# Performance work log

Hardware: AMD Instinct MI355X
Metric: run time of the kernel (lower is better)

The kernel has to match this reference:

```python
import jax, jax.numpy as jnp
import numpy as np

DIM = 2048
N_HEADS = 16
KV_LORA = 512
NOPE = 128
ROPE = 64
V_DIM = 128
QK_DIM = NOPE + ROPE  # 192
B, S = 2, 2048
ROPE_THETA = 10000.0
ROPE_FACTOR = 40.0
BETA_FAST, BETA_SLOW = 32, 1
ORIG_LEN, MAX_LEN = 4096, 16384
MSCALE_ARG = 1.0
EPS = 1e-6


def _precompute_freqs(seqlen):
    # DeepSeek YaRN-corrected rotary frequencies (interleaved-pair convention).
    d = ROPE
    freqs = 1.0 / (ROPE_THETA ** (np.arange(0, d, 2, dtype=np.float64) / d))
    if MAX_LEN > ORIG_LEN:
        def corr_dim(n_rot):
            return d * np.log(ORIG_LEN / (n_rot * 2 * np.pi)) / (2 * np.log(ROPE_THETA))
        low = max(int(np.floor(corr_dim(BETA_FAST))), 0)
        high = min(int(np.ceil(corr_dim(BETA_SLOW))), d - 1)
        smooth = 1.0 - np.clip((np.arange(d // 2) - low) / max(high - low, 1e-3), 0, 1)
        freqs = freqs / ROPE_FACTOR * (1 - smooth) + freqs * smooth
    t = np.arange(seqlen, dtype=np.float64)
    ang = np.outer(t, freqs)  # [S, d/2]
    return np.cos(ang).astype(np.float32), np.sin(ang).astype(np.float32)


def softmax_scale():
    scale = QK_DIM ** -0.5
    if MAX_LEN > ORIG_LEN:
        m = 0.1 * MSCALE_ARG * float(np.log(ROPE_FACTOR)) + 1.0
        scale = scale * m * m
    return scale


def setup_inputs() -> dict:
    key = jax.random.key(0)
    ks = jax.random.split(key, 6)
    w_std = 0.02
    fc, fs = _precompute_freqs(S)
    return {
        "x": jax.random.normal(ks[0], (B, S, DIM), jnp.float32),
        "wq": jax.random.normal(ks[1], (N_HEADS * QK_DIM, DIM), jnp.float32) * w_std,
        "wkv_a": jax.random.normal(ks[2], (KV_LORA + ROPE, DIM), jnp.float32) * w_std,
        "kv_norm_w": jnp.ones((KV_LORA,), jnp.float32),
        "wkv_b": jax.random.normal(ks[3], (N_HEADS * (NOPE + V_DIM), KV_LORA), jnp.float32) * w_std,
        "wo": jax.random.normal(ks[4], (DIM, N_HEADS * V_DIM), jnp.float32) * w_std,
        "freqs_cos": jnp.asarray(fc),
        "freqs_sin": jnp.asarray(fs),
    }


def _apply_rotary(x, cos, sin):
    # x: [B, S, H, d]; interleaved complex pairs, cos/sin: [S, d/2]
    xr = x.reshape(*x.shape[:-1], -1, 2)
    x_re, x_im = xr[..., 0], xr[..., 1]
    c = cos[None, :, None, :]
    s = sin[None, :, None, :]
    y_re = x_re * c - x_im * s
    y_im = x_re * s + x_im * c
    return jnp.stack((y_re, y_im), axis=-1).reshape(x.shape)


def _rmsnorm(x, w):
    return x * jax.lax.rsqrt(jnp.mean(x * x, axis=-1, keepdims=True) + EPS) * w


def reference(x, wq, wkv_a, kv_norm_w, wkv_b, wo, freqs_cos, freqs_sin):
    b, s, _ = x.shape
    # Q projection (q_lora_rank == 0 path)
    q = (x @ wq.T).reshape(b, s, N_HEADS, QK_DIM)
    q_nope, q_pe = q[..., :NOPE], q[..., NOPE:]
    q_pe = _apply_rotary(q_pe, freqs_cos, freqs_sin)
    # Low-rank KV compression
    kv = x @ wkv_a.T  # [B, S, 512+64]
    kv_c, k_pe = kv[..., :KV_LORA], kv[..., KV_LORA:]
    k_pe = _apply_rotary(k_pe[:, :, None, :], freqs_cos, freqs_sin)  # [B,S,1,64]
    kv_c = _rmsnorm(kv_c, kv_norm_w)
    kvb = (kv_c @ wkv_b.T).reshape(b, s, N_HEADS, NOPE + V_DIM)
    k_nope, v = kvb[..., :NOPE], kvb[..., NOPE:]
    k = jnp.concatenate([k_nope, jnp.broadcast_to(k_pe, (b, s, N_HEADS, ROPE))], axis=-1)
    # Causal attention
    scores = jnp.einsum("bshd,bthd->bhst", q, k) * softmax_scale()
    causal = jnp.tril(jnp.ones((s, s), bool))
    scores = jnp.where(causal[None, None], scores, jnp.float32(-1e30))
    p = jax.nn.softmax(scores, axis=-1)
    out = jnp.einsum("bhst,bthd->bshd", p, v).reshape(b, s, N_HEADS * V_DIM)
    return out @ wo.T
```

## Files before the change

### kernel.cpp

```cpp
#include <hip/hip_runtime.h>
#include <math.h>

#define NH      16
#define D_NOPE  128
#define D_ROPE  64
#define D_QK    192
#define D_V     128
#define KV_LORA 512
#define NB      2
#define SEQ     2048
#define NTOK    (NB*SEQ)
#define QROW    (NH*D_QK)
#define KVBROW  (NH*(D_NOPE+D_V))
#define EPSF    1e-6f

typedef unsigned short u16;
typedef float  floatx4 __attribute__((ext_vector_type(4)));
typedef __bf16 bf16x8  __attribute__((ext_vector_type(8)));
typedef u16    u16x4   __attribute__((ext_vector_type(4)));
typedef u16    u16x8   __attribute__((ext_vector_type(8)));

__device__ __forceinline__ u16 f2bf(float f) {
    unsigned u = __builtin_bit_cast(unsigned, f);
    return (u16)((u + 0x7fffu + ((u >> 16) & 1u)) >> 16);
}

__device__ __forceinline__ void async_copy16(const void* g, void* l) {
    __builtin_amdgcn_global_load_lds(
        (const __attribute__((address_space(1))) unsigned int*)g,
        (__attribute__((address_space(3))) unsigned int*)l,
        16, 0, 0);
}

__global__ __launch_bounds__(256) void cast_all(const float* __restrict__ x,
                                                const float* __restrict__ wq,
                                                const float* __restrict__ wkva,
                                                const float* __restrict__ wkvb,
                                                const float* __restrict__ wo,
                                                u16* __restrict__ xb,
                                                u16* __restrict__ wqb,
                                                u16* __restrict__ wkvab,
                                                u16* __restrict__ wkvbb,
                                                u16* __restrict__ wob) {
    int blk = blockIdx.x;
    const float* src; u16* dst; bool pad = false;
    if (blk < 8192)        { src = x;    dst = xb; }
    else if (blk < 14336)  { blk -= 8192;  src = wq;   dst = wqb; }
    else if (blk < 15616)  { blk -= 14336; src = wkva; dst = wkvab; pad = true; }
    else if (blk < 17664)  { blk -= 15616; src = wkvb; dst = wkvbb; }
    else                   { blk -= 17664; src = wo;   dst = wob; }
    const int i = (blk * 256 + threadIdx.x) * 4;
    u16x4 o;
    if (pad && (i >> 11) >= 576) {
        o[0] = 0; o[1] = 0; o[2] = 0; o[3] = 0;
    } else {
        const float4 v = *(const float4*)&src[i];
        o[0] = f2bf(v.x); o[1] = f2bf(v.y); o[2] = f2bf(v.z); o[3] = f2bf(v.w);
    }
    *(u16x4*)&dst[i] = o;
}

template<int MODE>
__global__ __launch_bounds__(256) void gemm_mfma(const u16* __restrict__ A,
                                                 const u16* __restrict__ B,
                                                 void* __restrict__ Cout,
                                                 u16* __restrict__ kbuf,
                                                 u16* __restrict__ vT,
                                                 int M, int N, int K) {
    __shared__ u16 As[128 * 32];
    __shared__ u16 Bs[128 * 32];
    const int tid  = threadIdx.x;
    const int wave = tid >> 6, lane = tid & 63;
    const int m0 = blockIdx.y * 128, n0 = blockIdx.x * 128;
    const int wm = (wave & 1) * 64, wn = (wave >> 1) * 64;

    const int srow = wave * 32 + (lane >> 2);
    const int kch  = (lane & 3) * 8;
    const u16* gA0 = A + (size_t)(m0 + srow) * K + kch;
    const u16* gA1 = gA0 + (size_t)16 * K;
    const u16* gB0 = B + (size_t)(n0 + srow) * K + kch;
    const u16* gB1 = gB0 + (size_t)16 * K;
    u16* lA0 = &As[(wave * 32) * 32];
    u16* lA1 = &As[(wave * 32 + 16) * 32];
    u16* lB0 = &Bs[(wave * 32) * 32];
    u16* lB1 = &Bs[(wave * 32 + 16) * 32];

    floatx4 acc[4][4];
#pragma unroll
    for (int i = 0; i < 4; ++i)
#pragma unroll
        for (int j = 0; j < 4; ++j) acc[i][j] = 0.f;

    const int lrow = lane & 15;
    const int lkh  = (lane >> 4) * 8;

    for (int k0 = 0; k0 < K; k0 += 32) {
        __syncthreads();
        async_copy16(gA0 + k0, lA0);
        async_copy16(gA1 + k0, lA1);
        async_copy16(gB0 + k0, lB0);
        async_copy16(gB1 + k0, lB1);
        __syncthreads();
        bf16x8 a[4], b[4];
#pragma unroll
        for (int mi = 0; mi < 4; ++mi)
            a[mi] = *(const bf16x8*)&As[(wm + mi * 16 + lrow) * 32 + lkh];
#pragma unroll
        for (int ni = 0; ni < 4; ++ni)
            b[ni] = *(const bf16x8*)&Bs[(wn + ni * 16 + lrow) * 32 + lkh];
#pragma unroll
        for (int mi = 0; mi < 4; ++mi)
#pragma unroll
            for (int ni = 0; ni < 4; ++ni)
                acc[mi][ni] = __builtin_amdgcn_mfma_f32_16x16x32_bf16(
                    a[mi], b[ni], acc[mi][ni], 0, 0, 0);
    }

    const int crow = (lane >> 4) * 4, ccol = lane & 15;
#pragma unroll
    for (int mi = 0; mi < 4; ++mi)
#pragma unroll
        for (int ni = 0; ni < 4; ++ni) {
            const int m = m0 + wm + mi * 16 + crow;
            const int c = n0 + wn + ni * 16 + ccol;
            if (MODE == 0) {
                float* cp = (float*)Cout + (size_t)m * N + c;
#pragma unroll
                for (int r = 0; r < 4; ++r) cp[(size_t)r * N] = acc[mi][ni][r];
            } else if (MODE == 1) {
                u16* cp = (u16*)Cout + (size_t)m * N + c;
#pragma unroll
                for (int r = 0; r < 4; ++r) cp[(size_t)r * N] = f2bf(acc[mi][ni][r]);
            } else {
                const int hh = c >> 8, j = c & 255;
                const int bb = m >> 11, t = m & 2047;
                if (j < 128) {
#pragma unroll
                    for (int r = 0; r < 4; ++r)
                        kbuf[(((size_t)hh * 2 + bb) * 2048 + t + r) * 192 + j] =
                            f2bf(acc[mi][ni][r]);
                } else {
                    u16x4 pk;
#pragma unroll
                    for (int r = 0; r < 4; ++r) pk[r] = f2bf(acc[mi][ni][r]);
                    *(u16x4*)&vT[(((size_t)hh * 2 + bb) * 128 + (j - 128)) * 2048 + t] = pk;
                }
            }
        }
}


__global__ __launch_bounds__(256) void kv_fix(const float* __restrict__ kv_raw,
                                              const float* __restrict__ w,
                                              const float* __restrict__ fcos,
                                              const float* __restrict__ fsin,
                                              u16* __restrict__ kvn_bf,
                                              u16* __restrict__ kbuf) {
    const int row = blockIdx.x;
    const int tid = threadIdx.x;
    const float* src = kv_raw + (size_t)row * 640;
    const float v0 = src[tid];
    const float v1 = src[256 + tid];
    float ss = v0 * v0 + v1 * v1;
#pragma unroll
    for (int off = 32; off > 0; off >>= 1) ss += __shfl_down(ss, off, 64);
    __shared__ float red[4];
    __shared__ float kpe_s[64];
    if ((tid & 63) == 0) red[tid >> 6] = ss;
    if (tid < 32) {
        const int s = row & (SEQ - 1);
        const float c  = fcos[s * 32 + tid];
        const float sn = fsin[s * 32 + tid];
        const float xr = src[KV_LORA + 2 * tid];
        const float xi = src[KV_LORA + 2 * tid + 1];
        kpe_s[2 * tid]     = xr * c - xi * sn;
        kpe_s[2 * tid + 1] = xr * sn + xi * c;
    }
    __syncthreads();
    const float tot = red[0] + red[1] + red[2] + red[3];
    const float inv = rsqrtf(tot * (1.0f / KV_LORA) + EPSF);
    kvn_bf[(size_t)row * KV_LORA + tid]       = f2bf(v0 * inv * w[tid]);
    kvn_bf[(size_t)row * KV_LORA + 256 + tid] = f2bf(v1 * inv * w[256 + tid]);
    const int bb = row >> 11, t = row & 2047;
    const int hh = tid >> 4, dg = (tid & 15) * 4;
    u16x4 pk;
#pragma unroll
    for (int j = 0; j < 4; ++j) pk[j] = f2bf(kpe_s[dg + j]);
    *(u16x4*)&kbuf[(((size_t)hh * 2 + bb) * 2048 + t) * 192 + 128 + dg] = pk;
}

__global__ __launch_bounds__(256, 2) void attn_mfma(const u16* __restrict__ qbf,
                                                    const u16* __restrict__ kbuf,
                                                    const u16* __restrict__ vT,
                                                    u16* __restrict__ att,
                                                    float scale) {
    __shared__ __attribute__((aligned(16))) u16 Ks[6 * 64 * 32];
    __shared__ __attribute__((aligned(16))) u16 Vs[2 * 128 * 32];
    __shared__ __attribute__((aligned(16))) u16 Ps[4][32 * 72];
    const int x = blockIdx.x;
    const int qt_base = (x & 1) ? (15 - (x >> 1)) : (x >> 1);
    const int qt = blockIdx.z ? (15 - qt_base) : qt_base;
    const int h = blockIdx.y, b = blockIdx.z;
    const int tid = threadIdx.x, wave = tid >> 6, lane = tid & 63;
    const int l15 = lane & 15, lg = lane >> 4;

    const u16* kb_base = kbuf + ((size_t)(h * 2 + b)) * 2048 * 192;
    const u16* vt_base = vT   + ((size_t)(h * 2 + b)) * 128 * 2048;

    int qrow[2];
    bf16x8 qf[2][6];
#pragma unroll
    for (int g = 0; g < 2; ++g) {
        qrow[g] = qt * 128 + g * 64 + wave * 16 + l15;
        const size_t qoff = ((size_t)(b * SEQ + qrow[g])) * QROW + h * 192 + lg * 8;
#pragma unroll
        for (int s = 0; s < 6; ++s) qf[g][s] = *(const bf16x8*)&qbf[qoff + s * 32];
    }

    floatx4 oacc[2][8];
#pragma unroll
    for (int g = 0; g < 2; ++g)
#pragma unroll
        for (int v = 0; v < 8; ++v) oacc[g][v] = 0.f;
    float m_run[2] = {-1e30f, -1e30f}, l_run[2] = {0.f, 0.f};

    const int kt_max = 2 * qt + 1;
    for (int kt = 0; kt <= kt_max; ++kt) {
        const int t0 = kt * 64;
        __syncthreads();
#pragma unroll
        for (int i = 0; i < 6; ++i) {
            const int base = (wave * 6 + i) * 64;
            const int slot = base + lane;
            const int s = slot >> 8, r = slot & 255, tk = r >> 2, ch = r & 3;
            async_copy16(kb_base + ((size_t)(t0 + tk)) * 192 + s * 32 + ch * 8,
                         &Ks[base * 8]);
        }
#pragma unroll
        for (int i = 0; i < 4; ++i) {
            const int base = (wave * 4 + i) * 64;
            const int slot = base + lane;
            const int s = slot >> 9, r = slot & 511, v = r >> 2, ch = r & 3;
            async_copy16(vt_base + ((size_t)v) * 2048 + t0 + s * 32 + ch * 8,
                         &Vs[base * 8]);
        }
        __syncthreads();
        floatx4 sacc[2][4];
#pragma unroll
        for (int g = 0; g < 2; ++g)
#pragma unroll
            for (int mt = 0; mt < 4; ++mt) sacc[g][mt] = 0.f;
#pragma unroll
        for (int s = 0; s < 6; ++s) {
#pragma unroll
            for (int mt = 0; mt < 4; ++mt) {
                const bf16x8 kf = *(const bf16x8*)&Ks[(s * 64 + mt * 16 + l15) * 32 + lg * 8];
#pragma unroll
                for (int g = 0; g < 2; ++g)
                    sacc[g][mt] = __builtin_amdgcn_mfma_f32_16x16x32_bf16(
                        kf, qf[g][s], sacc[g][mt], 0, 0, 0);
            }
        }
        float alpha[2];
#pragma unroll
        for (int g = 0; g < 2; ++g) {
            const bool full = (t0 + 63) <= (qt * 128 + g * 64 + wave * 16);
            float p[16];
            float tmax = -1e30f;
#pragma unroll
            for (int mt = 0; mt < 4; ++mt)
#pragma unroll
                for (int r = 0; r < 4; ++r) {
                    float v = sacc[g][mt][r] * scale;
                    if (!full) {
                        const int tglob = t0 + mt * 16 + lg * 4 + r;
                        v = (tglob <= qrow[g]) ? v : -1e30f;
                    }
                    p[mt * 4 + r] = v;
                    tmax = fmaxf(tmax, v);
                }
            tmax = fmaxf(tmax, __shfl_xor(tmax, 16));
            tmax = fmaxf(tmax, __shfl_xor(tmax, 32));
            const float mnew = fmaxf(m_run[g], tmax);
            alpha[g] = __expf(m_run[g] - mnew);
            m_run[g] = mnew;
            float rsum = 0.f;
#pragma unroll
            for (int k = 0; k < 16; ++k) { p[k] = __expf(p[k] - mnew); rsum += p[k]; }
            rsum += __shfl_xor(rsum, 16);
            rsum += __shfl_xor(rsum, 32);
            l_run[g] = l_run[g] * alpha[g] + rsum;
#pragma unroll
            for (int mt = 0; mt < 4; ++mt) {
                u16x4 pk;
#pragma unroll
                for (int r = 0; r < 4; ++r) pk[r] = f2bf(p[mt * 4 + r]);
                *(u16x4*)&Ps[wave][(g * 16 + l15) * 72 + mt * 16 + lg * 4] = pk;
            }
        }
#pragma unroll
        for (int g = 0; g < 2; ++g) {
            float af[4];
#pragma unroll
            for (int r = 0; r < 4; ++r) af[r] = __shfl(alpha[g], lg * 4 + r);
#pragma unroll
            for (int vt = 0; vt < 8; ++vt)
#pragma unroll
                for (int r = 0; r < 4; ++r) oacc[g][vt][r] *= af[r];
        }
#pragma unroll
        for (int s = 0; s < 2; ++s) {
            bf16x8 pf[2];
#pragma unroll
            for (int g = 0; g < 2; ++g)
                pf[g] = *(const bf16x8*)&Ps[wave][(g * 16 + l15) * 72 + s * 32 + lg * 8];
#pragma unroll
            for (int vt = 0; vt < 8; ++vt) {
                const bf16x8 vf = *(const bf16x8*)&Vs[(s * 128 + vt * 16 + l15) * 32 + lg * 8];
#pragma unroll
                for (int g = 0; g < 2; ++g)
                    oacc[g][vt] = __builtin_amdgcn_mfma_f32_16x16x32_bf16(
                        pf[g], vf, oacc[g][vt], 0, 0, 0);
            }
        }
    }
#pragma unroll
    for (int g = 0; g < 2; ++g) {
        float lf[4];
#pragma unroll
        for (int r = 0; r < 4; ++r) lf[r] = 1.0f / __shfl(l_run[g], lg * 4 + r);
#pragma unroll
        for (int vt = 0; vt < 8; ++vt)
#pragma unroll
            for (int r = 0; r < 4; ++r) {
                const int orow = b * SEQ + qt * 128 + g * 64 + wave * 16 + lg * 4 + r;
                att[(size_t)orow * 2048 + h * 128 + vt * 16 + l15] =
                    f2bf(oacc[g][vt][r] * lf[r]);
            }
    }
}

extern "C" void kernel_launch(void* const* d_in, const int* in_sizes, int n_in,
                              void* d_out, int out_size, void* d_ws, size_t ws_size,
                              hipStream_t stream) {
    const float* x     = (const float*)d_in[0];
    const float* wq    = (const float*)d_in[1];
    const float* wkv_a = (const float*)d_in[2];
    const float* knw   = (const float*)d_in[3];
    const float* wkv_b = (const float*)d_in[4];
    const float* wo    = (const float*)d_in[5];
    const float* fcos  = (const float*)d_in[6];
    const float* fsin  = (const float*)d_in[7];
    float* out = (float*)d_out;

    char* w = (char*)d_ws;
    u16*   x_bf    = (u16*)w;  w += (size_t)NTOK * 2048 * 2;
    u16*   wq_bf   = (u16*)w;  w += (size_t)QROW * 2048 * 2;
    u16*   wkva_bf = (u16*)w;  w += (size_t)640 * 2048 * 2;
    u16*   wkvb_bf = (u16*)w;  w += (size_t)KVBROW * KV_LORA * 2;
    u16*   wo_bf   = (u16*)w;  w += (size_t)2048 * 2048 * 2;
    u16*   q_bf    = (u16*)w;  w += (size_t)NTOK * QROW * 2;
    float* kv_raw  = (float*)w; w += (size_t)NTOK * 640 * 4;
    u16*   kvn_bf  = (u16*)w;  w += (size_t)NTOK * KV_LORA * 2;
    u16*   kbuf    = (u16*)w;  w += (size_t)NH * NB * SEQ * 192 * 2;
    u16*   vT      = (u16*)w;  w += (size_t)NH * NB * 128 * SEQ * 2;
    u16*   att_bf  = (u16*)w;  w += (size_t)NTOK * 2048 * 2;

    const double mm = 0.1 * 1.0 * log(40.0) + 1.0;
    const float scale = (float)((1.0 / sqrt((double)D_QK)) * mm * mm);

    dim3 blk(256);
    cast_all<<<dim3(21760), blk, 0, stream>>>(x, wq, wkv_a, wkv_b, wo,
                                              x_bf, wq_bf, wkva_bf, wkvb_bf, wo_bf);
    gemm_mfma<1><<<dim3(QROW / 128, NTOK / 128), blk, 0, stream>>>(
        x_bf, wq_bf, q_bf, nullptr, nullptr, NTOK, QROW, 2048);
    gemm_mfma<0><<<dim3(640 / 128, NTOK / 128), blk, 0, stream>>>(
        x_bf, wkva_bf, kv_raw, nullptr, nullptr, NTOK, 640, 2048);
    kv_fix<<<dim3(NTOK), blk, 0, stream>>>(kv_raw, knw, fcos, fsin, kvn_bf, kbuf);
    gemm_mfma<2><<<dim3(KVBROW / 128, NTOK / 128), blk, 0, stream>>>(
        kvn_bf, wkvb_bf, nullptr, kbuf, vT, NTOK, KVBROW, KV_LORA);
    attn_mfma<<<dim3(SEQ / 128, NH, NB), blk, 0, stream>>>(q_bf, kbuf, vT, att_bf, scale);
    gemm_mfma<0><<<dim3(2048 / 128, NTOK / 128), blk, 0, stream>>>(
        att_bf, wo_bf, out, nullptr, nullptr, NTOK, 2048, 2048);
}
```

Before: 443.7 us.

## Double-buffer K tiles in LDS and load V directly into registers

The attention kernel now double-buffers the K tile in shared memory, prefetching the next tile asynchronously while the current one is computed. V fragments are read straight from global memory into registers instead of being staged through LDS. s_setprio is raised around the MFMA sections. This removes one barrier per iteration and overlaps K loads with compute, but each wave now issues redundant global V loads and needs more registers, which could cut occupancy.

New measurement: 514.8 us. 1.16x slower.

```diff
diff --git a/kernel.cpp b/kernel.cpp
--- a/kernel.cpp
+++ b/kernel.cpp
@@ -194,8 +194,7 @@
                                                     const u16* __restrict__ vT,
                                                     u16* __restrict__ att,
                                                     float scale) {
-    __shared__ __attribute__((aligned(16))) u16 Ks[6 * 64 * 32];
-    __shared__ __attribute__((aligned(16))) u16 Vs[2 * 128 * 32];
+    __shared__ __attribute__((aligned(16))) u16 Ks[2][6 * 64 * 32];
     __shared__ __attribute__((aligned(16))) u16 Ps[4][32 * 72];
     const int x = blockIdx.x;
     const int qt_base = (x & 1) ? (15 - (x >> 1)) : (x >> 1);
@@ -224,43 +223,56 @@
         for (int v = 0; v < 8; ++v) oacc[g][v] = 0.f;
     float m_run[2] = {-1e30f, -1e30f}, l_run[2] = {0.f, 0.f};
 
-    const int kt_max = 2 * qt + 1;
-    for (int kt = 0; kt <= kt_max; ++kt) {
-        const int t0 = kt * 64;
-        __syncthreads();
+    auto stageK = [&](int bufi, int tt) {
 #pragma unroll
         for (int i = 0; i < 6; ++i) {
             const int base = (wave * 6 + i) * 64;
             const int slot = base + lane;
             const int s = slot >> 8, r = slot & 255, tk = r >> 2, ch = r & 3;
-            async_copy16(kb_base + ((size_t)(t0 + tk)) * 192 + s * 32 + ch * 8,
-                         &Ks[base * 8]);
-        }
-#pragma unroll
-        for (int i = 0; i < 4; ++i) {
-            const int base = (wave * 4 + i) * 64;
-            const int slot = base + lane;
-            const int s = slot >> 9, r = slot & 511, v = r >> 2, ch = r & 3;
-            async_copy16(vt_base + ((size_t)v) * 2048 + t0 + s * 32 + ch * 8,
-                         &Vs[base * 8]);
-        }
-        __syncthreads();
+            async_copy16(kb_base + ((size_t)(tt + tk)) * 192 + s * 32 + ch * 8,
+                         &Ks[bufi][base * 8]);
+        }
+    };
+
+    const int kt_max = 2 * qt + 1;
+    stageK(0, 0);
+    __syncthreads();
+
+    for (int kt = 0; kt <= kt_max; ++kt) {
+        const int t0 = kt * 64;
+        const int cur = kt & 1;
+
+        const u16* vrow = vt_base + (size_t)l15 * 2048 + t0 + lg * 8;
+        bf16x8 vregA[8], vregB[8];
+#pragma unroll
+        for (int vt = 0; vt < 8; ++vt)
+            vregA[vt] = *(const bf16x8*)&vrow[(size_t)vt * 16 * 2048];
+
+        if (kt < kt_max) stageK(cur ^ 1, t0 + 64);
+
         floatx4 sacc[2][4];
 #pragma unroll
         for (int g = 0; g < 2; ++g)
 #pragma unroll
             for (int mt = 0; mt < 4; ++mt) sacc[g][mt] = 0.f;
+        __builtin_amdgcn_s_setprio(1);
 #pragma unroll
         for (int s = 0; s < 6; ++s) {
 #pragma unroll
             for (int mt = 0; mt < 4; ++mt) {
-                const bf16x8 kf = *(const bf16x8*)&Ks[(s * 64 + mt * 16 + l15) * 32 + lg * 8];
+                const bf16x8 kf = *(const bf16x8*)&Ks[cur][(s * 64 + mt * 16 + l15) * 32 + lg * 8];
 #pragma unroll
                 for (int g = 0; g < 2; ++g)
                     sacc[g][mt] = __builtin_amdgcn_mfma_f32_16x16x32_bf16(
                         kf, qf[g][s], sacc[g][mt], 0, 0, 0);
             }
         }
+        __builtin_amdgcn_s_setprio(0);
+
+#pragma unroll
+        for (int vt = 0; vt < 8; ++vt)
+            vregB[vt] = *(const bf16x8*)&vrow[(size_t)vt * 16 * 2048 + 32];
+
         float alpha[2];
 #pragma unroll
         for (int g = 0; g < 2; ++g) {
@@ -308,6 +320,7 @@
 #pragma unroll
                 for (int r = 0; r < 4; ++r) oacc[g][vt][r] *= af[r];
         }
+        __builtin_amdgcn_s_setprio(1);
 #pragma unroll
         for (int s = 0; s < 2; ++s) {
             bf16x8 pf[2];
@@ -316,13 +329,16 @@
                 pf[g] = *(const bf16x8*)&Ps[wave][(g * 16 + l15) * 72 + s * 32 + lg * 8];
 #pragma unroll
             for (int vt = 0; vt < 8; ++vt) {
-                const bf16x8 vf = *(const bf16x8*)&Vs[(s * 128 + vt * 16 + l15) * 32 + lg * 8];
+                const bf16x8 vf = s ? vregB[vt] : vregA[vt];
 #pragma unroll
                 for (int g = 0; g < 2; ++g)
                     oacc[g][vt] = __builtin_amdgcn_mfma_f32_16x16x32_bf16(
                         pf[g], vf, oacc[g][vt], 0, 0, 0);
             }
         }
+        __builtin_amdgcn_s_setprio(0);
+
+        __syncthreads();
     }
 #pragma unroll
     for (int g = 0; g < 2; ++g) {
```

## Restructure attention into single-wave blocks reading K/V from global, with lazy rescaling

Applied to the files above, without the earlier changes.

Attention now runs one 64-thread wave per block, each handling 32 query rows, on a 32x64 grid ordered longest-first. K and V fragments are loaded straight from global memory (cache) instead of being staged cooperatively in LDS behind block barriers. It also adds a deferred online-softmax rescale that skips the output rescale unless the running max grows by more than 8. This removes syncthreads and LDS staging and raises block count, but each wave re-reads K/V without shared reuse, so global/L2 traffic rises and load latency is exposed.

Result: slower. 516.0 us (+16.3%).

```diff
diff --git a/kernel.cpp b/kernel.cpp
--- a/kernel.cpp
+++ b/kernel.cpp
@@ -189,30 +189,26 @@
     *(u16x4*)&kbuf[(((size_t)hh * 2 + bb) * 2048 + t) * 192 + 128 + dg] = pk;
 }
 
-__global__ __launch_bounds__(256, 2) void attn_mfma(const u16* __restrict__ qbf,
-                                                    const u16* __restrict__ kbuf,
-                                                    const u16* __restrict__ vT,
-                                                    u16* __restrict__ att,
-                                                    float scale) {
-    __shared__ __attribute__((aligned(16))) u16 Ks[6 * 64 * 32];
-    __shared__ __attribute__((aligned(16))) u16 Vs[2 * 128 * 32];
-    __shared__ __attribute__((aligned(16))) u16 Ps[4][32 * 72];
-    const int x = blockIdx.x;
-    const int qt_base = (x & 1) ? (15 - (x >> 1)) : (x >> 1);
-    const int qt = blockIdx.z ? (15 - qt_base) : qt_base;
-    const int h = blockIdx.y, b = blockIdx.z;
-    const int tid = threadIdx.x, wave = tid >> 6, lane = tid & 63;
+__global__ __launch_bounds__(64, 2) void attn_mfma(const u16* __restrict__ qbf,
+                                                   const u16* __restrict__ kbuf,
+                                                   const u16* __restrict__ vT,
+                                                   u16* __restrict__ att,
+                                                   float scale) {
+    __shared__ __attribute__((aligned(16))) u16 Ps[16 * 72];
+    const int hb = blockIdx.x;
+    const int c  = 63 - blockIdx.y;
+    const int h = hb >> 1, b = hb & 1;
+    const int lane = threadIdx.x;
     const int l15 = lane & 15, lg = lane >> 4;
 
-    const u16* kb_base = kbuf + ((size_t)(h * 2 + b)) * 2048 * 192;
-    const u16* vt_base = vT   + ((size_t)(h * 2 + b)) * 128 * 2048;
-
-    int qrow[2];
+    const u16* kb = kbuf + (size_t)hb * 2048 * 192;
+    const u16* vb = vT   + (size_t)hb * 128 * 2048;
+
+    const int qbase[2] = {32 * c, 32 * c + 16};
     bf16x8 qf[2][6];
 #pragma unroll
     for (int g = 0; g < 2; ++g) {
-        qrow[g] = qt * 128 + g * 64 + wave * 16 + l15;
-        const size_t qoff = ((size_t)(b * SEQ + qrow[g])) * QROW + h * 192 + lg * 8;
+        const size_t qoff = ((size_t)(b * SEQ + qbase[g] + l15)) * QROW + h * 192 + lg * 8;
 #pragma unroll
         for (int s = 0; s < 6; ++s) qf[g][s] = *(const bf16x8*)&qbf[qoff + s * 32];
     }
@@ -224,106 +220,91 @@
         for (int v = 0; v < 8; ++v) oacc[g][v] = 0.f;
     float m_run[2] = {-1e30f, -1e30f}, l_run[2] = {0.f, 0.f};
 
-    const int kt_max = 2 * qt + 1;
-    for (int kt = 0; kt <= kt_max; ++kt) {
-        const int t0 = kt * 64;
-        __syncthreads();
-#pragma unroll
-        for (int i = 0; i < 6; ++i) {
-            const int base = (wave * 6 + i) * 64;
-            const int slot = base + lane;
-            const int s = slot >> 8, r = slot & 255, tk = r >> 2, ch = r & 3;
-            async_copy16(kb_base + ((size_t)(t0 + tk)) * 192 + s * 32 + ch * 8,
-                         &Ks[base * 8]);
-        }
-#pragma unroll
-        for (int i = 0; i < 4; ++i) {
-            const int base = (wave * 4 + i) * 64;
-            const int slot = base + lane;
-            const int s = slot >> 9, r = slot & 511, v = r >> 2, ch = r & 3;
-            async_copy16(vt_base + ((size_t)v) * 2048 + t0 + s * 32 + ch * 8,
-                         &Vs[base * 8]);
-        }
-        __syncthreads();
-        floatx4 sacc[2][4];
-#pragma unroll
-        for (int g = 0; g < 2; ++g)
-#pragma unroll
-            for (int mt = 0; mt < 4; ++mt) sacc[g][mt] = 0.f;
-#pragma unroll
-        for (int s = 0; s < 6; ++s) {
+    const int nt = ((32 * c + 31) >> 6) + 1;
+
+    for (int kt = 0; kt < nt; ++kt) {
+        const int t0 = kt << 6;
+
+        floatx4 sacc0[4], sacc1[4];
+#pragma unroll
+        for (int mt = 0; mt < 4; ++mt) { sacc0[mt] = 0.f; sacc1[mt] = 0.f; }
+#pragma unroll
+        for (int s = 0; s < 6; ++s)
 #pragma unroll
             for (int mt = 0; mt < 4; ++mt) {
-                const bf16x8 kf = *(const bf16x8*)&Ks[(s * 64 + mt * 16 + l15) * 32 + lg * 8];
-#pragma unroll
-                for (int g = 0; g < 2; ++g)
-                    sacc[g][mt] = __builtin_amdgcn_mfma_f32_16x16x32_bf16(
-                        kf, qf[g][s], sacc[g][mt], 0, 0, 0);
-            }
-        }
-        float alpha[2];
+                const bf16x8 kf = *(const bf16x8*)&kb[(size_t)(t0 + mt * 16 + l15) * 192 + s * 32 + lg * 8];
+                sacc0[mt] = __builtin_amdgcn_mfma_f32_16x16x32_bf16(
+                    kf, qf[0][s], sacc0[mt], 0, 0, 0);
+                sacc1[mt] = __builtin_amdgcn_mfma_f32_16x16x32_bf16(
+                    kf, qf[1][s], sacc1[mt], 0, 0, 0);
+            }
+
+        bf16x8 pf[2][2];
 #pragma unroll
         for (int g = 0; g < 2; ++g) {
-            const bool full = (t0 + 63) <= (qt * 128 + g * 64 + wave * 16);
+            floatx4* sc = g ? sacc1 : sacc0;
+            const bool full = (t0 + 63) <= qbase[g];
             float p[16];
             float tmax = -1e30f;
 #pragma unroll
             for (int mt = 0; mt < 4; ++mt)
 #pragma unroll
                 for (int r = 0; r < 4; ++r) {
-                    float v = sacc[g][mt][r] * scale;
+                    float v = sc[mt][r] * scale;
                     if (!full) {
                         const int tglob = t0 + mt * 16 + lg * 4 + r;
-                        v = (tglob <= qrow[g]) ? v : -1e30f;
+                        v = (tglob <= qbase[g] + l15) ? v : -1e30f;
                     }
                     p[mt * 4 + r] = v;
                     tmax = fmaxf(tmax, v);
                 }
             tmax = fmaxf(tmax, __shfl_xor(tmax, 16));
             tmax = fmaxf(tmax, __shfl_xor(tmax, 32));
-            const float mnew = fmaxf(m_run[g], tmax);
-            alpha[g] = __expf(m_run[g] - mnew);
-            m_run[g] = mnew;
+            const bool defer = __all(tmax <= m_run[g] + 8.0f);
+            float mnew = m_run[g];
+            if (!defer) {
+                mnew = fmaxf(m_run[g], tmax);
+                const float alph = __expf(m_run[g] - mnew);
+                m_run[g] = mnew;
+                float af[4];
+#pragma unroll
+                for (int r = 0; r < 4; ++r) af[r] = __shfl(alph, lg * 4 + r);
+#pragma unroll
+                for (int vt = 0; vt < 8; ++vt)
+#pragma unroll
+                    for (int r = 0; r < 4; ++r) oacc[g][vt][r] *= af[r];
+                l_run[g] *= alph;
+            }
             float rsum = 0.f;
 #pragma unroll
             for (int k = 0; k < 16; ++k) { p[k] = __expf(p[k] - mnew); rsum += p[k]; }
             rsum += __shfl_xor(rsum, 16);
             rsum += __shfl_xor(rsum, 32);
-            l_run[g] = l_run[g] * alpha[g] + rsum;
+            l_run[g] += rsum;
 #pragma unroll
             for (int mt = 0; mt < 4; ++mt) {
                 u16x4 pk;
 #pragma unroll
                 for (int r = 0; r < 4; ++r) pk[r] = f2bf(p[mt * 4 + r]);
-                *(u16x4*)&Ps[wave][(g * 16 + l15) * 72 + mt * 16 + lg * 4] = pk;
-            }
+                *(u16x4*)&Ps[l15 * 72 + mt * 16 + lg * 4] = pk;
+            }
+#pragma unroll
+            for (int s = 0; s < 2; ++s)
+                pf[g][s] = *(const bf16x8*)&Ps[l15 * 72 + s * 32 + lg * 8];
         }
-#pragma unroll
-        for (int g = 0; g < 2; ++g) {
-            float af[4];
-#pragma unroll
-            for (int r = 0; r < 4; ++r) af[r] = __shfl(alpha[g], lg * 4 + r);
-#pragma unroll
-            for (int vt = 0; vt < 8; ++vt)
-#pragma unroll
-                for (int r = 0; r < 4; ++r) oacc[g][vt][r] *= af[r];
-        }
-#pragma unroll
-        for (int s = 0; s < 2; ++s) {
-            bf16x8 pf[2];
-#pragma unroll
-            for (int g = 0; g < 2; ++g)
-                pf[g] = *(const bf16x8*)&Ps[wave][(g * 16 + l15) * 72 + s * 32 + lg * 8];
+
+#pragma unroll
+        for (int s = 0; s < 2; ++s)
 #pragma unroll
             for (int vt = 0; vt < 8; ++vt) {
-                const bf16x8 vf = *(const bf16x8*)&Vs[(s * 128 + vt * 16 + l15) * 32 + lg * 8];
-#pragma unroll
-                for (int g = 0; g < 2; ++g)
-                    oacc[g][vt] = __builtin_amdgcn_mfma_f32_16x16x32_bf16(
-                        pf[g], vf, oacc[g][vt], 0, 0, 0);
-            }
-        }
-    }
+                const bf16x8 vf = *(const bf16x8*)&vb[(size_t)(vt * 16 + l15) * 2048 + t0 + s * 32 + lg * 8];
+                oacc[0][vt] = __builtin_amdgcn_mfma_f32_16x16x32_bf16(
+                    pf[0][s], vf, oacc[0][vt], 0, 0, 0);
+                oacc[1][vt] = __builtin_amdgcn_mfma_f32_16x16x32_bf16(
+                    pf[1][s], vf, oacc[1][vt], 0, 0, 0);
+            }
+    }
+
 #pragma unroll
     for (int g = 0; g < 2; ++g) {
         float lf[4];
@@ -333,7 +314,7 @@
         for (int vt = 0; vt < 8; ++vt)
 #pragma unroll
             for (int r = 0; r < 4; ++r) {
-                const int orow = b * SEQ + qt * 128 + g * 64 + wave * 16 + lg * 4 + r;
+                const int orow = b * SEQ + qbase[g] + lg * 4 + r;
                 att[(size_t)orow * 2048 + h * 128 + vt * 16 + l15] =
                     f2bf(oacc[g][vt][r] * lf[r]);
             }
@@ -379,7 +360,7 @@
     kv_fix<<<dim3(NTOK), blk, 0, stream>>>(kv_raw, knw, fcos, fsin, kvn_bf, kbuf);
     gemm_mfma<2><<<dim3(KVBROW / 128, NTOK / 128), blk, 0, stream>>>(
         kvn_bf, wkvb_bf, nullptr, kbuf, vT, NTOK, KVBROW, KV_LORA);
-    attn_mfma<<<dim3(SEQ / 128, NH, NB), blk, 0, stream>>>(q_bf, kbuf, vT, att_bf, scale);
+    attn_mfma<<<dim3(32, 64), dim3(64), 0, stream>>>(q_bf, kbuf, vT, att_bf, scale);
     gemm_mfma<0><<<dim3(2048 / 128, NTOK / 128), blk, 0, stream>>>(
         att_bf, wo_bf, out, nullptr, nullptr, NTOK, 2048, 2048);
 }
```
